# Kernel optimization log

Hardware: AMD Instinct MI355X
Metric: run time of the kernel (lower is better)

The kernel has to match this reference:

```python
import jax, jax.numpy as jnp
import numpy as np

V, T, H, N, HID = 512, 64, 256, 1024, 100
D = V + T  # biLSTM input dim


def _lstm_dir(x, Wih, Whh, b, reverse):
    # x: [n, Din]; PyTorch gate order i,f,g,o; b = b_ih + b_hh (equivalent math)
    xw = x @ Wih.T + b  # [n, 4H] precomputed input projection
    if reverse:
        xw = xw[::-1]
    h_dim = Whh.shape[1]

    def step(carry, xt):
        h, c = carry
        g = xt + h @ Whh.T
        i, f, gg, o = jnp.split(g, 4, axis=-1)
        i = jax.nn.sigmoid(i)
        f = jax.nn.sigmoid(f)
        gg = jnp.tanh(gg)
        o = jax.nn.sigmoid(o)
        c = f * c + i * gg
        h = o * jnp.tanh(c)
        return (h, c), h

    init = (jnp.zeros((h_dim,), x.dtype), jnp.zeros((h_dim,), x.dtype))
    _, hs = jax.lax.scan(step, init, xw)
    return hs[::-1] if reverse else hs


def setup_inputs() -> dict:
    key = jax.random.key(0)
    ks = jax.random.split(key, 20)
    s = 1.0 / np.sqrt(H)  # PyTorch LSTM init scale
    inp = {
        "word_table": jax.random.normal(ks[0], (V, V), jnp.float32) * 0.1,
        "pos_table": jax.random.normal(ks[1], (T, T), jnp.float32) * 0.1,
        # layer 0 fwd/bwd
        "l0f_Wih": jax.random.uniform(ks[2], (4 * H, D), jnp.float32, -s, s),
        "l0f_Whh": jax.random.uniform(ks[3], (4 * H, H), jnp.float32, -s, s),
        "l0f_b": jax.random.uniform(ks[4], (4 * H,), jnp.float32, -s, s),
        "l0b_Wih": jax.random.uniform(ks[5], (4 * H, D), jnp.float32, -s, s),
        "l0b_Whh": jax.random.uniform(ks[6], (4 * H, H), jnp.float32, -s, s),
        "l0b_b": jax.random.uniform(ks[7], (4 * H,), jnp.float32, -s, s),
        # layer 1 fwd/bwd (input = 2H)
        "l1f_Wih": jax.random.uniform(ks[8], (4 * H, 2 * H), jnp.float32, -s, s),
        "l1f_Whh": jax.random.uniform(ks[9], (4 * H, H), jnp.float32, -s, s),
        "l1f_b": jax.random.uniform(ks[10], (4 * H,), jnp.float32, -s, s),
        "l1b_Wih": jax.random.uniform(ks[11], (4 * H, 2 * H), jnp.float32, -s, s),
        "l1b_Whh": jax.random.uniform(ks[12], (4 * H, H), jnp.float32, -s, s),
        "l1b_b": jax.random.uniform(ks[13], (4 * H,), jnp.float32, -s, s),
        # edge-scorer MLP: Linear(4H,100) -> tanh -> Linear(100,1)
        "mlp_W1": jax.random.uniform(ks[14], (HID, 4 * H), jnp.float32, -0.03, 0.03),
        "mlp_b1": jax.random.uniform(ks[15], (HID,), jnp.float32, -0.03, 0.03),
        "mlp_W2": jax.random.uniform(ks[16], (1, HID), jnp.float32, -0.1, 0.1),
        "mlp_b2": jax.random.uniform(ks[17], (1,), jnp.float32, -0.1, 0.1),
        "word_idx": jax.random.randint(ks[18], (1, N), 0, V),
        "pos_idx": jax.random.randint(ks[19], (1, N), 0, T),
    }
    return inp


def reference(word_table, pos_table,
              l0f_Wih, l0f_Whh, l0f_b, l0b_Wih, l0b_Whh, l0b_b,
              l1f_Wih, l1f_Whh, l1f_b, l1b_Wih, l1b_Whh, l1b_b,
              mlp_W1, mlp_b1, mlp_W2, mlp_b2,
              word_idx, pos_idx):
    # embedding lookups on external tables, cat word+pos -> [n, D]
    x = jnp.concatenate([word_table[word_idx[0]], pos_table[pos_idx[0]]], axis=-1)
    # 2-layer bidirectional LSTM, batch=1 (squeezed)
    h = jnp.concatenate([_lstm_dir(x, l0f_Wih, l0f_Whh, l0f_b, False),
                         _lstm_dir(x, l0b_Wih, l0b_Whh, l0b_b, True)], axis=-1)  # [n, 2H]
    h = jnp.concatenate([_lstm_dir(h, l1f_Wih, l1f_Whh, l1f_b, False),
                         _lstm_dir(h, l1b_Wih, l1b_Whh, l1b_b, True)], axis=-1)  # [n, 2H]
    # pairwise edge scorer: layer_2(tanh(layer_1(cat(h_head, h_mod))))
    # split W1 = [Wh | Wm] so the cat never materializes per pair
    two_h = h.shape[-1]
    Wh, Wm = mlp_W1[:, :two_h], mlp_W1[:, two_h:]
    A = h @ Wh.T  # [n, HID] head contribution
    B = h @ Wm.T  # [n, HID] modifier contribution
    hid = jnp.tanh(A[:, None, :] + B[None, :, :] + mlp_b1)  # [n, n, HID]
    scores = hid @ mlp_W2[0] + mlp_b2[0]  # [n, n]
    n = scores.shape[0]
    eye = jnp.eye(n, dtype=bool)
    scores = jnp.where(eye, 0.0, scores)  # diagonal left at 0, as in the torch loop
    return jax.nn.softmax(scores, axis=0)
```

## Files before the change

### kernel.cpp

```cpp
#include <hip/hip_runtime.h>
#include <hip/hip_bf16.h>


#define L2E 1.4426950408889634f

__device__ __forceinline__ float fast_rcp(float x) { return __builtin_amdgcn_rcpf(x); }
__device__ __forceinline__ float sigm_f(float x) {
    return fast_rcp(1.f + exp2f(-x * L2E));
}
__device__ __forceinline__ float tanh_f(float x) {
    return 1.f - 2.f * fast_rcp(1.f + exp2f(x * (2.f * L2E)));
}

__device__ __forceinline__ void st_msg(unsigned long long* p, unsigned long long m) {
    asm volatile("global_store_dwordx2 %0, %1, off sc0 sc1"
                 :: "v"(p), "v"(m) : "memory");
}

__device__ __forceinline__ unsigned long long poll_msg(
    const unsigned long long* p, unsigned want)
{
    unsigned long long r0, r1, r2, r3, r = 0;
    bool done = false;
    for (int it = 0; it < 8192 && !done; ++it) {
        asm volatile(
            "global_load_dwordx2 %0, %4, off sc0 sc1\n\t"
            "global_load_dwordx2 %1, %4, off sc0 sc1\n\t"
            "global_load_dwordx2 %2, %4, off sc0 sc1\n\t"
            "global_load_dwordx2 %3, %4, off sc0 sc1\n\t"
            "s_waitcnt vmcnt(3)"
            : "=&v"(r0), "=&v"(r1), "=&v"(r2), "=&v"(r3)
            : "v"(p) : "memory");
        if (__all((unsigned)(r0 >> 32) == want)) { r = r0; done = true; }
        if (!done) {
            asm volatile("s_waitcnt vmcnt(2)" ::: "memory");
            if (__all((unsigned)(r1 >> 32) == want)) { r = r1; done = true; }
        }
        if (!done) {
            asm volatile("s_waitcnt vmcnt(1)" ::: "memory");
            if (__all((unsigned)(r2 >> 32) == want)) { r = r2; done = true; }
        }
        if (!done) {
            asm volatile("s_waitcnt vmcnt(0)" ::: "memory");
            if (__all((unsigned)(r3 >> 32) == want)) { r = r3; done = true; }
        }
        asm volatile("s_waitcnt vmcnt(0)" ::: "memory");
    }
    if (!done) {
        do {
            r = __hip_atomic_load(p, __ATOMIC_RELAXED, __HIP_MEMORY_SCOPE_AGENT);
        } while (!__all((unsigned)(r >> 32) == want));
    }
    return r;
}

__global__ __launch_bounds__(256) void embed_kernel(
    const float* __restrict__ wt, const float* __restrict__ pt,
    const int* __restrict__ wi, const int* __restrict__ pi,
    float* __restrict__ x)
{
    int idx = blockIdx.x * 256 + threadIdx.x;
    if (idx >= 1024 * 576) return;
    int n = idx / 576, c = idx % 576;
    x[idx] = (c < 512) ? wt[wi[n] * 512 + c] : pt[pi[n] * 64 + (c - 512)];
}

__global__ __launch_bounds__(256) void gemm_bias(
    const float* __restrict__ A,
    const float* __restrict__ W0, const float* __restrict__ W1,
    const float* __restrict__ b0, const float* __restrict__ b1,
    float* __restrict__ C0, float* __restrict__ C1,
    int M, int N, int K)
{
    const float* W = blockIdx.z ? W1 : W0;
    const float* bias = blockIdx.z ? b1 : b0;
    float* C = blockIdx.z ? C1 : C0;
    int m0 = blockIdx.y * 64, n0 = blockIdx.x * 64;
    __shared__ float As[16][65];
    __shared__ float Ws[16][65];
    int tid = threadIdx.x;
    int tx = tid & 15, ty = tid >> 4;
    float acc[4][4] = {};
    int lr = tid >> 2, lkc = (tid & 3) * 4;
    for (int k0 = 0; k0 < K; k0 += 16) {
        float4 a4 = *(const float4*)&A[(size_t)(m0 + lr) * K + k0 + lkc];
        float4 w4 = *(const float4*)&W[(size_t)(n0 + lr) * K + k0 + lkc];
        As[lkc + 0][lr] = a4.x; As[lkc + 1][lr] = a4.y;
        As[lkc + 2][lr] = a4.z; As[lkc + 3][lr] = a4.w;
        Ws[lkc + 0][lr] = w4.x; Ws[lkc + 1][lr] = w4.y;
        Ws[lkc + 2][lr] = w4.z; Ws[lkc + 3][lr] = w4.w;
        __syncthreads();
#pragma unroll
        for (int k = 0; k < 16; k++) {
            float a[4], b[4];
#pragma unroll
            for (int i = 0; i < 4; i++) a[i] = As[k][ty * 4 + i];
#pragma unroll
            for (int j = 0; j < 4; j++) b[j] = Ws[k][tx * 4 + j];
#pragma unroll
            for (int i = 0; i < 4; i++)
#pragma unroll
                for (int j = 0; j < 4; j++) acc[i][j] += a[i] * b[j];
        }
        __syncthreads();
    }
    int colbase = n0 + tx * 4;
    float4 bv = *(const float4*)&bias[colbase];
#pragma unroll
    for (int i = 0; i < 4; i++) {
        float4 o;
        o.x = acc[i][0] + bv.x; o.y = acc[i][1] + bv.y;
        o.z = acc[i][2] + bv.z; o.w = acc[i][3] + bv.w;
        *(float4*)&C[(size_t)(m0 + ty * 4 + i) * N + colbase] = o;
    }
}

__global__ __launch_bounds__(512, 2) void lstm_scan(
    const float* __restrict__ xw_f, const float* __restrict__ xw_b,
    const float* __restrict__ Whh_f, const float* __restrict__ Whh_b,
    float* __restrict__ hout,
    unsigned long long* __restrict__ hx)
{
    const int sub  = blockIdx.x;
    const int tid  = threadIdx.x;
    const int lane = tid & 63;
    const int wv   = tid >> 6;
    const int dsel = tid >> 8;
    const int tl   = tid & 255;
    const int q    = tl >> 6;
    const int lr   = tl & 63;
    const int R    = (lr >> 4) * 256 + sub * 16 + (lr & 15);

    const float* __restrict__ Whh = dsel ? Whh_b : Whh_f;

    float4 w4[16];
    {
        const float4* Wr = (const float4*)(Whh + (size_t)R * 256 + (q << 6));
#pragma unroll
        for (int i = 0; i < 16; i++) w4[i] = Wr[i];
    }

    __shared__ float h0_sh[256], h1_sh[256];
    __shared__ float part0[256], part1[256];
    float* __restrict__ h_shd = dsel ? h1_sh : h0_sh;
    float* __restrict__ partd = dsel ? part1 : part0;

    const bool isProd = (wv == 0) && (lane < 32);
    float c = 0.f;
    if (tid < 256) { h0_sh[tid] = 0.f; h1_sh[tid] = 0.f; }
    __syncthreads();

    for (int t = 0; t < 1024; t++) {
        float xg0 = 0.f, xg1 = 0.f, xg2 = 0.f, xg3 = 0.f;
        if (isProd) {
            int pd = lane >> 4, hid = lane & 15;
            int trp = pd ? (1023 - t) : t;
            const float* xr = (pd ? xw_b : xw_f) +
                              (size_t)trp * 1024 + sub * 16 + hid;
            xg0 = xr[0];   xg1 = xr[256];
            xg2 = xr[512]; xg3 = xr[768];
        }

        float a0 = 0.f, a1 = 0.f, a2 = 0.f, a3 = 0.f;
        const float4* hp4 = (const float4*)&h_shd[q << 6];
#pragma unroll
        for (int i = 0; i < 16; i += 4) {
            float4 h0v = hp4[i + 0], h1v = hp4[i + 1];
            float4 h2v = hp4[i + 2], h3v = hp4[i + 3];
            a0 += w4[i+0].x*h0v.x + w4[i+0].y*h0v.y + w4[i+0].z*h0v.z + w4[i+0].w*h0v.w;
            a1 += w4[i+1].x*h1v.x + w4[i+1].y*h1v.y + w4[i+1].z*h1v.z + w4[i+1].w*h1v.w;
            a2 += w4[i+2].x*h2v.x + w4[i+2].y*h2v.y + w4[i+2].z*h2v.z + w4[i+2].w*h2v.w;
            a3 += w4[i+3].x*h3v.x + w4[i+3].y*h3v.y + w4[i+3].z*h3v.z + w4[i+3].w*h3v.w;
        }
        partd[tl] = (a0 + a1) + (a2 + a3);
        __syncthreads();

        const int par = (t + 1) & 1;
        if (isProd) {
            int pd = lane >> 4, hid = lane & 15;
            const float* pp = pd ? part1 : part0;
            float s0 = pp[hid]       + pp[64 + hid]  + pp[128 + hid]  + pp[192 + hid]  + xg0;
            float s1 = pp[16 + hid]  + pp[80 + hid]  + pp[144 + hid]  + pp[208 + hid]  + xg1;
            float s2 = pp[32 + hid]  + pp[96 + hid]  + pp[160 + hid]  + pp[224 + hid]  + xg2;
            float s3 = pp[48 + hid]  + pp[112 + hid] + pp[176 + hid]  + pp[240 + hid]  + xg3;
            float iv = sigm_f(s0), fv = sigm_f(s1);
            float gv = tanh_f(s2), ov = sigm_f(s3);
            c = fv * c + iv * gv;
            float h = ov * tanh_f(c);
            if (t + 1 < 1024) {
                unsigned long long msg =
                    ((unsigned long long)(unsigned)(t + 1) << 32) |
                    (unsigned long long)__float_as_uint(h);
                st_msg(&hx[(((sub << 1) + par) << 5) + lane], msg);
                (pd ? h1_sh : h0_sh)[sub * 16 + hid] = h;
            }
            int trp = pd ? (1023 - t) : t;
            hout[(size_t)trp * 512 + (pd << 8) + sub * 16 + hid] = h;
        }
        if (t + 1 < 1024 && (wv != 0 || lane >= 32)) {
            int pw = (wv == 0) ? ((sub + 8) & 15)
                               : ((lane < 32) ? ((sub + wv) & 15)
                                              : ((sub + wv + 8) & 15));
            const unsigned long long* sp =
                &hx[(((pw << 1) + par) << 5) + (lane & 31)];
            unsigned long long v = poll_msg(sp, (unsigned)(t + 1));
            float hv = __uint_as_float((unsigned)v);
            int hl = lane & 31;
            ((hl < 16) ? h0_sh : h1_sh)[pw * 16 + (hl & 15)] = hv;
        }
        __syncthreads();

#pragma unroll
        for (int i = 0; i < 16; i++)
            asm volatile("" : "+v"(w4[i].x), "+v"(w4[i].y),
                              "+v"(w4[i].z), "+v"(w4[i].w));
    }
}

__global__ __launch_bounds__(256) void transpose_w1(
    const float* __restrict__ W1, float* __restrict__ W1T)
{
    int idx = blockIdx.x * 256 + threadIdx.x;
    if (idx >= 100 * 1024) return;
    int n = idx / 1024, j = idx % 1024;
    W1T[j * 100 + n] = W1[idx];
}

__global__ __launch_bounds__(256) void ab_kernel(
    const float* __restrict__ h1, const float* __restrict__ W1T,
    const float* __restrict__ b1v,
    float* __restrict__ Ab, float* __restrict__ Bb)
{
    int m0 = blockIdx.x * 16;
    __shared__ float hs[16][512];
    int tid = threadIdx.x;
    for (int idx = tid * 4; idx < 16 * 512; idx += 1024) {
        int r = idx >> 9, cc = idx & 511;
        *(float4*)&hs[r][cc] = *(const float4*)&h1[(size_t)(m0 + r) * 512 + cc];
    }
    __syncthreads();
    bool isB = tid >= 128;
    int n = tid & 127;
    if (n < 100) {
        float acc[16] = {};
        const float* wbase = W1T + (isB ? 512 * 100 : 0) + n;
#pragma unroll 4
        for (int k = 0; k < 512; k++) {
            float wv = wbase[k * 100];
#pragma unroll
            for (int m = 0; m < 16; m++) acc[m] += hs[m][k] * wv;
        }
        float badd = isB ? 0.f : b1v[n];
        float* dst = isB ? Bb : Ab;
#pragma unroll
        for (int m = 0; m < 16; m++) dst[(m0 + m) * 100 + n] = acc[m] + badd;
    }
}

__global__ __launch_bounds__(256) void pair_kernel(
    const float* __restrict__ Ab, const float* __restrict__ Bb,
    const float* __restrict__ W2, const float* __restrict__ b2,
    float* __restrict__ sT)
{
    int i0 = blockIdx.x * 32, j0 = blockIdx.y * 32;
    __shared__ float Ash[32][101];
    __shared__ float Bsh[32][101];
    __shared__ float w2s[100];
    int tid = threadIdx.x;
    for (int idx = tid; idx < 3200; idx += 256) {
        int r = idx / 100, cc = idx % 100;
        Ash[r][cc] = Ab[(i0 + r) * 100 + cc];
        Bsh[r][cc] = Bb[(j0 + r) * 100 + cc];
    }
    if (tid < 100) w2s[tid] = W2[tid];
    __syncthreads();
    float b2v = b2[0];
    int il = (tid & 15) * 2, jl = (tid >> 4) * 2;
    float a00 = 0.f, a01 = 0.f, a10 = 0.f, a11 = 0.f;
#pragma unroll 4
    for (int k = 0; k < 100; k++) {
        float wv = w2s[k];
        float x0 = Ash[il][k], x1 = Ash[il + 1][k];
        float y0 = Bsh[jl][k], y1 = Bsh[jl + 1][k];
        a00 += wv * tanh_f(x0 + y0);
        a01 += wv * tanh_f(x0 + y1);
        a10 += wv * tanh_f(x1 + y0);
        a11 += wv * tanh_f(x1 + y1);
    }
    float vals[2][2] = {{a00, a01}, {a10, a11}};
#pragma unroll
    for (int a = 0; a < 2; a++)
#pragma unroll
        for (int b = 0; b < 2; b++) {
            int gi2 = i0 + il + a, gj = j0 + jl + b;
            float v = vals[a][b] + b2v;
            if (gi2 == gj) v = 0.f;
            sT[(size_t)gj * 1024 + gi2] = v;
        }
}

__global__ __launch_bounds__(256) void colstats(
    const float* __restrict__ sT, float* __restrict__ mx, float* __restrict__ rs)
{
    int j = blockIdx.x;
    const float* row = sT + (size_t)j * 1024;
    int tid = threadIdx.x;
    __shared__ float red[256];
    float m = -INFINITY;
    for (int i = tid; i < 1024; i += 256) m = fmaxf(m, row[i]);
    red[tid] = m; __syncthreads();
    for (int s = 128; s > 0; s >>= 1) {
        if (tid < s) red[tid] = fmaxf(red[tid], red[tid + s]);
        __syncthreads();
    }
    float mxv = red[0];
    __syncthreads();
    float ssum = 0.f;
    for (int i = tid; i < 1024; i += 256) ssum += exp2f((row[i] - mxv) * L2E);
    red[tid] = ssum; __syncthreads();
    for (int s = 128; s > 0; s >>= 1) {
        if (tid < s) red[tid] += red[tid + s];
        __syncthreads();
    }
    if (tid == 0) { mx[j] = mxv; rs[j] = 1.f / red[0]; }
}

__global__ __launch_bounds__(256) void writeout(
    const float* __restrict__ sT, const float* __restrict__ mx,
    const float* __restrict__ rs, float* __restrict__ out)
{
    int i0 = blockIdx.x * 32, j0 = blockIdx.y * 32;
    __shared__ float til[32][33];
    int tid = threadIdx.x;
    int r = tid >> 3, c4 = (tid & 7) * 4;
    float4 v = *(const float4*)&sT[(size_t)(j0 + r) * 1024 + i0 + c4];
    til[r][c4 + 0] = v.x; til[r][c4 + 1] = v.y;
    til[r][c4 + 2] = v.z; til[r][c4 + 3] = v.w;
    __syncthreads();
    float4 o;
    float* op = &out[(size_t)(i0 + r) * 1024 + j0 + c4];
    o.x = exp2f((til[c4 + 0][r] - mx[j0 + c4 + 0]) * L2E) * rs[j0 + c4 + 0];
    o.y = exp2f((til[c4 + 1][r] - mx[j0 + c4 + 1]) * L2E) * rs[j0 + c4 + 1];
    o.z = exp2f((til[c4 + 2][r] - mx[j0 + c4 + 2]) * L2E) * rs[j0 + c4 + 2];
    o.w = exp2f((til[c4 + 3][r] - mx[j0 + c4 + 3]) * L2E) * rs[j0 + c4 + 3];
    *(float4*)op = o;
}

extern "C" void kernel_launch(void* const* d_in, const int* in_sizes, int n_in,
                              void* d_out, int out_size, void* d_ws, size_t ws_size,
                              hipStream_t stream)
{
    const float* word_table = (const float*)d_in[0];
    const float* pos_table  = (const float*)d_in[1];
    const float* l0f_Wih = (const float*)d_in[2];
    const float* l0f_Whh = (const float*)d_in[3];
    const float* l0f_b   = (const float*)d_in[4];
    const float* l0b_Wih = (const float*)d_in[5];
    const float* l0b_Whh = (const float*)d_in[6];
    const float* l0b_b   = (const float*)d_in[7];
    const float* l1f_Wih = (const float*)d_in[8];
    const float* l1f_Whh = (const float*)d_in[9];
    const float* l1f_b   = (const float*)d_in[10];
    const float* l1b_Wih = (const float*)d_in[11];
    const float* l1b_Whh = (const float*)d_in[12];
    const float* l1b_b   = (const float*)d_in[13];
    const float* mlp_W1  = (const float*)d_in[14];
    const float* mlp_b1  = (const float*)d_in[15];
    const float* mlp_W2  = (const float*)d_in[16];
    const float* mlp_b2  = (const float*)d_in[17];
    const int*   word_idx = (const int*)d_in[18];
    const int*   pos_idx  = (const int*)d_in[19];
    float* out = (float*)d_out;

    float* ws = (float*)d_ws;
    const size_t OFF_X   = 0;
    const size_t OFF_XWF = 589824;
    const size_t OFF_XWB = 1638400;
    const size_t OFF_H0  = 2686976;
    const size_t OFF_H1  = 3211264;
    const size_t OFF_W1T = 3735552;
    const size_t OFF_A   = 3837952;
    const size_t OFF_B   = 3940352;
    const size_t OFF_ST  = 4042752;
    const size_t OFF_MX  = 5091328;
    const size_t OFF_RS  = 5092352;
    const size_t OFF_HX  = 5095424;

    float* x   = ws + OFF_X;
    float* xwf = ws + OFF_XWF;
    float* xwb = ws + OFF_XWB;
    float* h0  = ws + OFF_H0;
    float* h1  = ws + OFF_H1;
    float* w1t = ws + OFF_W1T;
    float* Ab  = ws + OFF_A;
    float* Bb  = ws + OFF_B;
    float* sT  = ws + OFF_ST;
    float* mx  = ws + OFF_MX;
    float* rs  = ws + OFF_RS;
    unsigned long long* hx0 = (unsigned long long*)(ws + OFF_HX);
    unsigned long long* hx1 = hx0 + 1024;

    hipMemsetAsync(hx0, 0, 2048 * sizeof(unsigned long long), stream);

    embed_kernel<<<(1024 * 576 + 255) / 256, 256, 0, stream>>>(
        word_table, pos_table, word_idx, pos_idx, x);

    transpose_w1<<<(100 * 1024 + 255) / 256, 256, 0, stream>>>(mlp_W1, w1t);

    gemm_bias<<<dim3(16, 16, 2), 256, 0, stream>>>(
        x, l0f_Wih, l0b_Wih, l0f_b, l0b_b, xwf, xwb, 1024, 1024, 576);

    lstm_scan<<<16, 512, 0, stream>>>(
        xwf, xwb, l0f_Whh, l0b_Whh, h0, hx0);

    gemm_bias<<<dim3(16, 16, 2), 256, 0, stream>>>(
        h0, l1f_Wih, l1b_Wih, l1f_b, l1b_b, xwf, xwb, 1024, 1024, 512);

    lstm_scan<<<16, 512, 0, stream>>>(
        xwf, xwb, l1f_Whh, l1b_Whh, h1, hx1);

    ab_kernel<<<64, 256, 0, stream>>>(h1, w1t, mlp_b1, Ab, Bb);

    pair_kernel<<<dim3(32, 32), 256, 0, stream>>>(Ab, Bb, mlp_W2, mlp_b2, sT);

    colstats<<<1024, 256, 0, stream>>>(sT, mx, rs);

    writeout<<<dim3(32, 32), 256, 0, stream>>>(sT, mx, rs, out);
}
```

Baseline: 3.718 ms.

## Split LSTM recurrence across 32 blocks with wave-shuffle reduction and double-buffered h

The persistent LSTM scan now runs on 32 workgroups instead of 16, so each thread keeps half as many recurrent weights in registers (8 float4 instead of 16). Gate partial sums are reduced inside the wave with shuffles instead of going through shared memory and an extra barrier, which leaves one __syncthreads per timestep. Shared h is double-buffered and padded to avoid bank conflicts, and the next step's input projection is prefetched. The cost is twice as many cross-block messages to poll per step, and a four-slot parity mailbox is used to avoid overwrites.

```diff
diff --git a/kernel.cpp b/kernel.cpp
--- a/kernel.cpp
+++ b/kernel.cpp
@@ -125,46 +125,56 @@
     const int tid  = threadIdx.x;
     const int lane = tid & 63;
     const int wv   = tid >> 6;
-    const int dsel = tid >> 8;
-    const int tl   = tid & 255;
-    const int q    = tl >> 6;
-    const int lr   = tl & 63;
-    const int R    = (lr >> 4) * 256 + sub * 16 + (lr & 15);
-
-    const float* __restrict__ Whh = dsel ? Whh_b : Whh_f;
-
-    float4 w4[16];
+    const int d    = wv >> 2;
+    const int hp   = wv & 3;
+    const int r    = lane >> 3;
+    const int kc   = lane & 7;
+    const int g    = r >> 1, hh = r & 1;
+    const int hid  = hp * 2 + hh;
+    const int R    = g * 256 + sub * 8 + hid;
+
+    const float* __restrict__ Whh = d ? Whh_b : Whh_f;
+    const float* __restrict__ xwd = d ? xw_b : xw_f;
+
+    float4 w4[8];
     {
-        const float4* Wr = (const float4*)(Whh + (size_t)R * 256 + (q << 6));
-#pragma unroll
-        for (int i = 0; i < 16; i++) w4[i] = Wr[i];
-    }
-
-    __shared__ float h0_sh[256], h1_sh[256];
-    __shared__ float part0[256], part1[256];
-    float* __restrict__ h_shd = dsel ? h1_sh : h0_sh;
-    float* __restrict__ partd = dsel ? part1 : part0;
-
-    const bool isProd = (wv == 0) && (lane < 32);
+        const float4* Wr = (const float4*)(Whh + (size_t)R * 256 + (kc << 5));
+#pragma unroll
+        for (int i = 0; i < 8; i++) w4[i] = Wr[i];
+    }
+
+    __shared__ float h0s[2][288], h1s[2][288];
+
+    const bool isLead = (lane < 2);
     float c = 0.f;
-    if (tid < 256) { h0_sh[tid] = 0.f; h1_sh[tid] = 0.f; }
+    float xg0 = 0.f, xg1 = 0.f, xg2 = 0.f, xg3 = 0.f;
+    if (isLead) {
+        int trow0 = d ? 1023 : 0;
+        const float* xr = xwd + (size_t)trow0 * 1024 + sub * 8 + hp * 2 + lane;
+        xg0 = xr[0]; xg1 = xr[256]; xg2 = xr[512]; xg3 = xr[768];
+    }
+
+    int pw = 0, v = 0;
+    if (!isLead) {
+        int p = wv * 62 + (lane - 2);
+        pw = (sub + 1 + (p >> 4)) & 31;
+        v  = p & 15;
+    }
+
+    if (tid < 288) {
+        h0s[0][tid] = 0.f; h0s[1][tid] = 0.f;
+        h1s[0][tid] = 0.f; h1s[1][tid] = 0.f;
+    }
     __syncthreads();
 
     for (int t = 0; t < 1024; t++) {
-        float xg0 = 0.f, xg1 = 0.f, xg2 = 0.f, xg3 = 0.f;
-        if (isProd) {
-            int pd = lane >> 4, hid = lane & 15;
-            int trp = pd ? (1023 - t) : t;
-            const float* xr = (pd ? xw_b : xw_f) +
-                              (size_t)trp * 1024 + sub * 16 + hid;
-            xg0 = xr[0];   xg1 = xr[256];
-            xg2 = xr[512]; xg3 = xr[768];
-        }
-
+        const int par  = t & 1;
+        const int parn = (t + 1) & 1;
+
+        const float4* hp4 = (const float4*)((d ? h1s[par] : h0s[par]) + kc * 36);
         float a0 = 0.f, a1 = 0.f, a2 = 0.f, a3 = 0.f;
-        const float4* hp4 = (const float4*)&h_shd[q << 6];
-#pragma unroll
-        for (int i = 0; i < 16; i += 4) {
+#pragma unroll
+        for (int i = 0; i < 8; i += 4) {
             float4 h0v = hp4[i + 0], h1v = hp4[i + 1];
             float4 h2v = hp4[i + 2], h3v = hp4[i + 3];
             a0 += w4[i+0].x*h0v.x + w4[i+0].y*h0v.y + w4[i+0].z*h0v.z + w4[i+0].w*h0v.w;
@@ -172,48 +182,46 @@
             a2 += w4[i+2].x*h2v.x + w4[i+2].y*h2v.y + w4[i+2].z*h2v.z + w4[i+2].w*h2v.w;
             a3 += w4[i+3].x*h3v.x + w4[i+3].y*h3v.y + w4[i+3].z*h3v.z + w4[i+3].w*h3v.w;
         }
-        partd[tl] = (a0 + a1) + (a2 + a3);
-        __syncthreads();
-
-        const int par = (t + 1) & 1;
-        if (isProd) {
-            int pd = lane >> 4, hid = lane & 15;
-            const float* pp = pd ? part1 : part0;
-            float s0 = pp[hid]       + pp[64 + hid]  + pp[128 + hid]  + pp[192 + hid]  + xg0;
-            float s1 = pp[16 + hid]  + pp[80 + hid]  + pp[144 + hid]  + pp[208 + hid]  + xg1;
-            float s2 = pp[32 + hid]  + pp[96 + hid]  + pp[160 + hid]  + pp[224 + hid]  + xg2;
-            float s3 = pp[48 + hid]  + pp[112 + hid] + pp[176 + hid]  + pp[240 + hid]  + xg3;
-            float iv = sigm_f(s0), fv = sigm_f(s1);
-            float gv = tanh_f(s2), ov = sigm_f(s3);
+        float acc = (a0 + a1) + (a2 + a3);
+
+        acc += __shfl_xor(acc, 1);
+        acc += __shfl_xor(acc, 2);
+        acc += __shfl_xor(acc, 4);
+        int hsel = lane & 1;
+        float s0 = __shfl(acc, (0 * 2 + hsel) * 8);
+        float s1 = __shfl(acc, (1 * 2 + hsel) * 8);
+        float s2 = __shfl(acc, (2 * 2 + hsel) * 8);
+        float s3 = __shfl(acc, (3 * 2 + hsel) * 8);
+
+        if (isLead) {
+            float iv = sigm_f(s0 + xg0), fv = sigm_f(s1 + xg1);
+            float gv = tanh_f(s2 + xg2), ov = sigm_f(s3 + xg3);
             c = fv * c + iv * gv;
             float h = ov * tanh_f(c);
+            int myhid = hp * 2 + lane;
+            int G = sub * 8 + myhid;
+            int trow = d ? (1023 - t) : t;
             if (t + 1 < 1024) {
                 unsigned long long msg =
                     ((unsigned long long)(unsigned)(t + 1) << 32) |
                     (unsigned long long)__float_as_uint(h);
-                st_msg(&hx[(((sub << 1) + par) << 5) + lane], msg);
-                (pd ? h1_sh : h0_sh)[sub * 16 + hid] = h;
+                st_msg(&hx[((sub << 2) + ((t + 1) & 3)) * 16 + d * 8 + myhid], msg);
+                (d ? h1s[parn] : h0s[parn])[(G >> 5) * 36 + (G & 31)] = h;
+                int trown = d ? (1022 - t) : (t + 1);
+                const float* xr = xwd + (size_t)trown * 1024 + G;
+                xg0 = xr[0]; xg1 = xr[256]; xg2 = xr[512]; xg3 = xr[768];
             }
-            int trp = pd ? (1023 - t) : t;
-            hout[(size_t)trp * 512 + (pd << 8) + sub * 16 + hid] = h;
-        }
-        if (t + 1 < 1024 && (wv != 0 || lane >= 32)) {
-            int pw = (wv == 0) ? ((sub + 8) & 15)
-                               : ((lane < 32) ? ((sub + wv) & 15)
-                                              : ((sub + wv + 8) & 15));
+            hout[(size_t)trow * 512 + (d << 8) + G] = h;
+        }
+        if (!isLead && t + 1 < 1024) {
             const unsigned long long* sp =
-                &hx[(((pw << 1) + par) << 5) + (lane & 31)];
-            unsigned long long v = poll_msg(sp, (unsigned)(t + 1));
-            float hv = __uint_as_float((unsigned)v);
-            int hl = lane & 31;
-            ((hl < 16) ? h0_sh : h1_sh)[pw * 16 + (hl & 15)] = hv;
+                &hx[((pw << 2) + ((t + 1) & 3)) * 16 + v];
+            unsigned long long mv = poll_msg(sp, (unsigned)(t + 1));
+            float hv = __uint_as_float((unsigned)mv);
+            int G = pw * 8 + (v & 7);
+            ((v >> 3) ? h1s[parn] : h0s[parn])[(G >> 5) * 36 + (G & 31)] = hv;
         }
         __syncthreads();
-
-#pragma unroll
-        for (int i = 0; i < 16; i++)
-            asm volatile("" : "+v"(w4[i].x), "+v"(w4[i].y),
-                              "+v"(w4[i].z), "+v"(w4[i].w));
     }
 }
 
@@ -398,9 +406,9 @@
     float* mx  = ws + OFF_MX;
     float* rs  = ws + OFF_RS;
     unsigned long long* hx0 = (unsigned long long*)(ws + OFF_HX);
-    unsigned long long* hx1 = hx0 + 1024;
-
-    hipMemsetAsync(hx0, 0, 2048 * sizeof(unsigned long long), stream);
+    unsigned long long* hx1 = hx0 + 2048;
+
+    hipMemsetAsync(hx0, 0, 4096 * sizeof(unsigned long long), stream);
 
     embed_kernel<<<(1024 * 576 + 255) / 256, 256, 0, stream>>>(
         word_table, pos_table, word_idx, pos_idx, x);
@@ -410,13 +418,13 @@
     gemm_bias<<<dim3(16, 16, 2), 256, 0, stream>>>(
         x, l0f_Wih, l0b_Wih, l0f_b, l0b_b, xwf, xwb, 1024, 1024, 576);
 
-    lstm_scan<<<16, 512, 0, stream>>>(
+    lstm_scan<<<32, 512, 0, stream>>>(
         xwf, xwb, l0f_Whh, l0b_Whh, h0, hx0);
 
     gemm_bias<<<dim3(16, 16, 2), 256, 0, stream>>>(
         h0, l1f_Wih, l1b_Wih, l1f_b, l1b_b, xwf, xwb, 1024, 1024, 512);
 
-    lstm_scan<<<16, 512, 0, stream>>>(
+    lstm_scan<<<32, 512, 0, stream>>>(
         xwf, xwb, l1f_Whh, l1b_Whh, h1, hx1);
 
     ab_kernel<<<64, 256, 0, stream>>>(h1, w1t, mlp_b1, Ab, Bb);
```

After: 5.731 ms. +54.2%, slower.
